# Optimization experiments

Measured on AMD Instinct MI355X. Metric: run time of the kernel, lower is better.

## Reference

```python
import math
import jax, jax.numpy as jnp
import numpy as np


def _tril_colmajor_index(d):
    # Maps packed icf tail entries (column-by-column, strictly lower) to (r, c).
    idx = np.zeros((d, d), dtype=np.int32)
    p = 0
    for c in range(d):
        for r in range(c + 1, d):
            idx[r, c] = p
            p += 1
    mask = np.tri(d, d, -1, dtype=bool)  # strictly lower triangular
    return idx, mask


def setup_inputs() -> dict:
    key = jax.random.key(0)
    k1, k2, k3, k4 = jax.random.split(key, 4)
    K, d, N = 64, 32, 50000
    icf_cols = d + d * (d - 1) // 2  # 528
    return {
        "alphas": jax.random.normal(k1, (K,), dtype=jnp.float32),
        "means": jax.random.normal(k2, (K, d), dtype=jnp.float32),
        "icf": jax.random.normal(k3, (K, icf_cols), dtype=jnp.float32),
        "x": jax.random.normal(k4, (N, d), dtype=jnp.float32),
        "wishart_gamma": jnp.ones((), dtype=jnp.float32),
        "wishart_m": jnp.ones((), dtype=jnp.float32),
    }


def reference(alphas, means, icf, x, wishart_gamma, wishart_m):
    n, d = x.shape
    k = alphas.shape[0]
    idx, mask = _tril_colmajor_index(d)
    idx = jnp.asarray(idx)
    mask = jnp.asarray(mask)

    Qdiags = jnp.exp(icf[:, :d])            # [K, d]
    sum_qs = jnp.sum(icf[:, :d], axis=1)    # [K]
    Ltail = icf[:, d:]                      # [K, d(d-1)/2]
    # Vectorized constructL: strictly-lower triangular L per component. [K, d, d]
    L = jnp.where(mask[None], Ltail[:, idx], jnp.zeros((), icf.dtype))

    xc = x[:, None, :] - means[None, :, :]  # [N, K, d]
    # Qtimesx: diag scaling + batched triangular matvec
    Lx = Qdiags[None] * xc + jnp.einsum('kij,nkj->nki', L, xc)  # [N, K, d]
    sqsum = jnp.sum(Lx * Lx, axis=2)        # [N, K]

    inner = alphas[None, :] + sum_qs[None, :] - 0.5 * sqsum
    slse = jnp.sum(jax.scipy.special.logsumexp(inner, axis=1))

    CONSTANT = -n * d * 0.5 * math.log(2 * math.pi)

    # log_wishart_prior
    nw = d + wishart_m + 1.0
    out_w = jnp.sum(0.5 * wishart_gamma * wishart_gamma
                    * (jnp.sum(Qdiags ** 2, axis=1) + jnp.sum(Ltail ** 2, axis=1))
                    - wishart_m * sum_qs)
    C = nw * d * jnp.log(wishart_gamma / math.sqrt(2.0))
    prior = out_w - k * (C - jax.scipy.special.multigammaln(0.5 * nw, d))

    return CONSTANT + slse - n * jax.scipy.special.logsumexp(alphas) + prior
```

## Files before the change

kernel.cpp:

```cpp
#include <hip/hip_runtime.h>
#include <math.h>
#include <utility>

#define K_COMP 64
#define D 32
#define NTRIL 496
#define ICF_COLS 528
#define NPAIR 528
#define NFEAT 560
#define NCHUNK 18
#define PTS_PER_BLK 32
#define ROWB 1168

typedef __attribute__((ext_vector_type(8))) short v8s;
typedef __attribute__((ext_vector_type(4))) float v4f;

__device__ __forceinline__ unsigned short f2bf(float f) {
  unsigned int u = __float_as_uint(f);
  unsigned int r = (u + 0x7FFFu + ((u >> 16) & 1u)) >> 16;
  return (unsigned short)r;
}
__device__ __forceinline__ v8s asv8(int4 v) {
  union { int4 i; v8s s; } u; u.i = v; return u.s;
}

constexpr int pr_i(int t) { int i = 0; while (t >= D - i) { t -= D - i; ++i; } return i; }
constexpr int pr_j(int t) { int i = 0; while (t >= D - i) { t -= D - i; ++i; } return i + t; }

template<int F> __device__ __forceinline__ float feat(const float (&xr)[D]) {
  if constexpr (F < 32) return xr[F];
  else if constexpr (F < NFEAT) {
    constexpr int t = F - 32, i = pr_i(t), j = pr_j(t);
    return xr[i] * xr[j];
  } else return 0.0f;
}

template<int F0> __device__ __forceinline__ void write4(const float (&xr)[D], char* row) {
  unsigned int d0 = (unsigned int)f2bf(feat<F0+0>(xr)) | ((unsigned int)f2bf(feat<F0+1>(xr)) << 16);
  unsigned int d1 = (unsigned int)f2bf(feat<F0+2>(xr)) | ((unsigned int)f2bf(feat<F0+3>(xr)) << 16);
  *reinterpret_cast<uint2*>(row + (size_t)F0 * 2) = make_uint2(d0, d1);
}
template<int BASE, size_t... Qs> __device__ __forceinline__
void gen72(const float (&xr)[D], char* row, std::index_sequence<Qs...>) {
  (write4<BASE + 4 * (int)Qs>(xr, row), ...);
}

__global__ __launch_bounds__(64) void gmm_prep(
    const float* __restrict__ alphas, const float* __restrict__ means,
    const float* __restrict__ icf, const float* __restrict__ wg,
    const float* __restrict__ wm,
    uint4* __restrict__ Whi, float* __restrict__ eSa, float* __restrict__ wwk)
{
  int k = blockIdx.x;
  int l = threadIdx.x;
  __shared__ float M[D][D + 1];
  __shared__ float mu[D], b[D], v[D];
  __shared__ float At[NPAIR];
  __shared__ float red[64];

  const float* ick = icf + (size_t)k * ICF_COLS;

  if (l < D) {
    mu[l] = means[k * D + l];
    float q = __expf(ick[l]);
    for (int c = 0; c < D; ++c) {
      float val;
      if (c < l) { int off = c * 31 - c * (c - 1) / 2; val = ick[D + off + (l - c - 1)]; }
      else if (c == l) val = q;
      else val = 0.0f;
      M[l][c] = val;
    }
  }
  __syncthreads();
  if (l < D) {
    float acc = 0.f;
    for (int c = 0; c < D; ++c) acc = fmaf(M[l][c], mu[c], acc);
    b[l] = acc;
  }
  __syncthreads();
  if (l < D) {
    float acc = 0.f;
    for (int r = 0; r < D; ++r) acc = fmaf(M[r][l], b[r], acc);
    v[l] = acc;
  }
  for (int t = l; t < NPAIR; t += 64) {
    int tt = t, i = 0;
    while (tt >= D - i) { tt -= D - i; ++i; }
    int j = i + tt;
    float acc = 0.f;
    for (int r = 0; r < D; ++r) acc = fmaf(M[r][i], M[r][j], acc);
    At[t] = (i == j) ? -0.5f * acc : -acc;
  }
  float part = 0.f;
  for (int e = l; e < D * D; e += 64) {
    float mv = M[e / D][e % D];
    part = fmaf(mv, mv, part);
  }
  red[l] = part;
  __syncthreads();
  for (int st = 32; st > 0; st >>= 1) {
    if (l < st) red[l] += red[l + st];
    __syncthreads();
  }
  if (l == 0) {
    float msq = red[0];
    float sumq = 0.f;
    for (int i = 0; i < D; ++i) sumq += ick[i];
    float bsq = 0.f;
    for (int i = 0; i < D; ++i) bsq = fmaf(b[i], b[i], bsq);
    eSa[k] = alphas[k] + sumq - 0.5f * bsq;
    float g = wg[0], mm = wm[0];
    wwk[k] = 0.5f * g * g * msq - mm * sumq;
  }
  __syncthreads();

  int s = k >> 4, krow = k & 15;
  for (int u = l; u < NCHUNK * 4; u += 64) {
    int c = u >> 2, g = u & 3;
    unsigned int hw[4] = {0, 0, 0, 0};
    for (int j2 = 0; j2 < 8; ++j2) {
      int f = c * 32 + g * 8 + j2;
      float wv2;
      if (f < 32) wv2 = v[f];
      else if (f < NFEAT) wv2 = At[f - 32];
      else wv2 = 0.0f;
      hw[j2 >> 1] |= ((unsigned int)f2bf(wv2)) << (16 * (j2 & 1));
    }
    Whi[(s * NCHUNK + c) * 64 + g * 16 + krow] = make_uint4(hw[0], hw[1], hw[2], hw[3]);
  }
}

__global__ __launch_bounds__(256) void gmm_main(
    const float* __restrict__ x, const int4* __restrict__ Whi,
    const float* __restrict__ eSa, int N, float* __restrict__ partials)
{
  __shared__ __align__(16) char phi[PTS_PER_BLK * ROWB];
  __shared__ float lmm[4][PTS_PER_BLK];
  __shared__ float lss[4][PTS_PER_BLK];

  int tid = threadIdx.x;
  int lane = tid & 63;

  {
    int ptl = tid & 31;
    int h = tid >> 5;
    int n = blockIdx.x * PTS_PER_BLK + ptl;
    int nn = (n < N) ? n : (N - 1);
    float xr[D];
    const float4* xp = reinterpret_cast<const float4*>(x + (size_t)nn * D);
#pragma unroll
    for (int i = 0; i < D / 4; ++i) {
      float4 vv = xp[i];
      xr[4 * i + 0] = vv.x; xr[4 * i + 1] = vv.y; xr[4 * i + 2] = vv.z; xr[4 * i + 3] = vv.w;
    }
    char* row = phi + (size_t)ptl * ROWB;
    switch (h) {
      case 0: gen72<  0>(xr, row, std::make_index_sequence<18>{}); break;
      case 1: gen72< 72>(xr, row, std::make_index_sequence<18>{}); break;
      case 2: gen72<144>(xr, row, std::make_index_sequence<18>{}); break;
      case 3: gen72<216>(xr, row, std::make_index_sequence<18>{}); break;
      case 4: gen72<288>(xr, row, std::make_index_sequence<18>{}); break;
      case 5: gen72<360>(xr, row, std::make_index_sequence<18>{}); break;
      case 6: gen72<432>(xr, row, std::make_index_sequence<18>{}); break;
      case 7: gen72<504>(xr, row, std::make_index_sequence<18>{}); break;
    }
  }
  __syncthreads();

  int slice = __builtin_amdgcn_readfirstlane(tid >> 6);
  int g = lane >> 4, n16 = lane & 15;

  v4f acc0 = {0.f, 0.f, 0.f, 0.f};
  v4f acc1 = {0.f, 0.f, 0.f, 0.f};
  const char* brow0 = phi + (size_t)(0 * 16 + n16) * ROWB + g * 16;
  const char* brow1 = phi + (size_t)(1 * 16 + n16) * ROWB + g * 16;

#pragma unroll
  for (int c = 0; c < NCHUNK; ++c) {
    int4 ah = Whi[(slice * NCHUNK + c) * 64 + lane];
    int4 b0 = *reinterpret_cast<const int4*>(brow0 + c * 64);
    int4 b1 = *reinterpret_cast<const int4*>(brow1 + c * 64);
    v8s ahs = asv8(ah), b0s = asv8(b0), b1s = asv8(b1);
    acc0 = __builtin_amdgcn_mfma_f32_16x16x32_bf16(ahs, b0s, acc0, 0, 0, 0);
    acc1 = __builtin_amdgcn_mfma_f32_16x16x32_bf16(ahs, b1s, acc1, 0, 0, 0);
  }

  float4 es = reinterpret_cast<const float4*>(eSa)[slice * 4 + (lane >> 4)];
  acc0.x += es.x; acc0.y += es.y; acc0.z += es.z; acc0.w += es.w;
  acc1.x += es.x; acc1.y += es.y; acc1.z += es.z; acc1.w += es.w;

#pragma unroll
  for (int G = 0; G < 2; ++G) {
    v4f a = (G == 0) ? acc0 : acc1;
    float m = fmaxf(fmaxf(a.x, a.y), fmaxf(a.z, a.w));
    float sv = __expf(a.x - m) + __expf(a.y - m) + __expf(a.z - m) + __expf(a.w - m);
#pragma unroll
    for (int off = 16; off <= 32; off <<= 1) {
      float mo = __shfl_xor(m, off);
      float so = __shfl_xor(sv, off);
      float mn = fmaxf(m, mo);
      sv = sv * __expf(m - mn) + so * __expf(mo - mn);
      m = mn;
    }
    if (lane < 16) { lmm[slice][G * 16 + lane] = m; lss[slice][G * 16 + lane] = sv; }
  }
  __syncthreads();

  if (tid < PTS_PER_BLK) {
    float m0 = lmm[0][tid], m1 = lmm[1][tid], m2 = lmm[2][tid], m3 = lmm[3][tid];
    float mm = fmaxf(fmaxf(m0, m1), fmaxf(m2, m3));
    float ss = lss[0][tid] * __expf(m0 - mm) + lss[1][tid] * __expf(m1 - mm)
             + lss[2][tid] * __expf(m2 - mm) + lss[3][tid] * __expf(m3 - mm);
    int n = blockIdx.x * PTS_PER_BLK + tid;
    float lse = (n < N) ? (mm + __logf(ss)) : 0.f;
#pragma unroll
    for (int off = 16; off > 0; off >>= 1) lse += __shfl_down(lse, off);
    if (tid == 0) partials[blockIdx.x] = lse;
  }
}

__global__ __launch_bounds__(256) void gmm_final(
    const float* __restrict__ wwk, const float* __restrict__ partials, int nblocks,
    const float* __restrict__ alphas, const float* __restrict__ wg,
    const float* __restrict__ wm, int N, float* __restrict__ out)
{
  int tid = threadIdx.x;
  __shared__ double sd[256];
  __shared__ float samax;
  __shared__ double s_slse, s_sa, s_ow;

  double acc = 0.0;
  for (int i = tid; i < nblocks; i += 256) acc += (double)partials[i];
  sd[tid] = acc;
  __syncthreads();
  for (int st = 128; st > 0; st >>= 1) {
    if (tid < st) sd[tid] += sd[tid + st];
    __syncthreads();
  }
  if (tid == 0) s_slse = sd[0];
  __syncthreads();

  if (tid < 64) {
    float m = alphas[tid];
#pragma unroll
    for (int off = 32; off > 0; off >>= 1) m = fmaxf(m, __shfl_xor(m, off));
    if (tid == 0) samax = m;
  }
  __syncthreads();

  sd[tid] = (tid < K_COMP) ? exp((double)(alphas[tid] - samax)) : 0.0;
  __syncthreads();
  for (int st = 128; st > 0; st >>= 1) {
    if (tid < st) sd[tid] += sd[tid + st];
    __syncthreads();
  }
  if (tid == 0) s_sa = sd[0];
  __syncthreads();

  sd[tid] = (tid < K_COMP) ? (double)wwk[tid] : 0.0;
  __syncthreads();
  for (int st = 128; st > 0; st >>= 1) {
    if (tid < st) sd[tid] += sd[tid + st];
    __syncthreads();
  }
  if (tid == 0) s_ow = sd[0];
  __syncthreads();

  double nw = (double)D + (double)wm[0] + 1.0;
  sd[tid] = (tid < D) ? lgamma(0.5 * nw + (1.0 - (double)(tid + 1)) * 0.5) : 0.0;
  __syncthreads();
  for (int st = 128; st > 0; st >>= 1) {
    if (tid < st) sd[tid] += sd[tid + st];
    __syncthreads();
  }

  if (tid == 0) {
    double mg = (D * (D - 1) / 4.0) * log(M_PI) + sd[0];
    double lse_a = (double)samax + log(s_sa);
    double g = (double)wg[0];
    double C = nw * (double)D * log(g / sqrt(2.0));
    double CONST = -(double)N * D * 0.5 * log(2.0 * M_PI);
    double prior = s_ow - (double)K_COMP * (C - mg);
    out[0] = (float)(CONST + s_slse - (double)N * lse_a + prior);
  }
}

extern "C" void kernel_launch(void* const* d_in, const int* in_sizes, int n_in,
                              void* d_out, int out_size, void* d_ws, size_t ws_size,
                              hipStream_t stream)
{
  const float* alphas = (const float*)d_in[0];
  const float* means  = (const float*)d_in[1];
  const float* icf    = (const float*)d_in[2];
  const float* x      = (const float*)d_in[3];
  const float* wg     = (const float*)d_in[4];
  const float* wm     = (const float*)d_in[5];
  float* out = (float*)d_out;

  int N = in_sizes[3] / D;
  int npblk = (N + PTS_PER_BLK - 1) / PTS_PER_BLK;

  char* wsb = (char*)d_ws;
  const size_t WBYTES = (size_t)4 * NCHUNK * 64 * 16;
  uint4* Whi = (uint4*)wsb;
  float* eSa = (float*)(wsb + WBYTES);
  float* wwk = eSa + K_COMP;
  float* partials = wwk + K_COMP;

  gmm_prep<<<K_COMP, 64, 0, stream>>>(alphas, means, icf, wg, wm, Whi, eSa, wwk);
  gmm_main<<<npblk, 256, 0, stream>>>(x, (const int4*)Whi, eSa, N, partials);
  gmm_final<<<1, 256, 0, stream>>>(wwk, partials, npblk, alphas, wg, wm, N, out);
}
```

Measured before the change: 42.29 us.

## Build quadratic features in registers with full symmetric Gram matrix per wave

Replaces the shared-memory packed upper-triangle feature table with on-the-fly generation of x_a*x_b products in registers, using the full symmetric 32x32 matrix (scaled by -0.5) plus a linear chunk, for 33 K-chunks. Each wave now handles 32 points against all 64 components (4 slices), so the cross-wave LDS logsumexp reduction and block barrier go away, and A fragments are software-prefetched from global. This removes LDS traffic and syncs at the cost of nearly double the MFMA work (33 vs 18 chunks per slice) and per-chunk scalar x loads.

```diff
diff --git a/kernel.cpp b/kernel.cpp
--- a/kernel.cpp
+++ b/kernel.cpp
@@ -1,16 +1,11 @@
 #include <hip/hip_runtime.h>
 #include <math.h>
-#include <utility>
 
 #define K_COMP 64
 #define D 32
-#define NTRIL 496
 #define ICF_COLS 528
-#define NPAIR 528
-#define NFEAT 560
-#define NCHUNK 18
-#define PTS_PER_BLK 32
-#define ROWB 1168
+#define NCH 33
+#define SLICES 4
 
 typedef __attribute__((ext_vector_type(8))) short v8s;
 typedef __attribute__((ext_vector_type(4))) float v4f;
@@ -20,42 +15,25 @@
   unsigned int r = (u + 0x7FFFu + ((u >> 16) & 1u)) >> 16;
   return (unsigned short)r;
 }
+__device__ __forceinline__ v8s pack8(unsigned a, unsigned b, unsigned c, unsigned d) {
+  union { unsigned u[4]; v8s s; } u;
+  u.u[0] = a; u.u[1] = b; u.u[2] = c; u.u[3] = d; return u.s;
+}
 __device__ __forceinline__ v8s asv8(int4 v) {
   union { int4 i; v8s s; } u; u.i = v; return u.s;
-}
-
-constexpr int pr_i(int t) { int i = 0; while (t >= D - i) { t -= D - i; ++i; } return i; }
-constexpr int pr_j(int t) { int i = 0; while (t >= D - i) { t -= D - i; ++i; } return i + t; }
-
-template<int F> __device__ __forceinline__ float feat(const float (&xr)[D]) {
-  if constexpr (F < 32) return xr[F];
-  else if constexpr (F < NFEAT) {
-    constexpr int t = F - 32, i = pr_i(t), j = pr_j(t);
-    return xr[i] * xr[j];
-  } else return 0.0f;
-}
-
-template<int F0> __device__ __forceinline__ void write4(const float (&xr)[D], char* row) {
-  unsigned int d0 = (unsigned int)f2bf(feat<F0+0>(xr)) | ((unsigned int)f2bf(feat<F0+1>(xr)) << 16);
-  unsigned int d1 = (unsigned int)f2bf(feat<F0+2>(xr)) | ((unsigned int)f2bf(feat<F0+3>(xr)) << 16);
-  *reinterpret_cast<uint2*>(row + (size_t)F0 * 2) = make_uint2(d0, d1);
-}
-template<int BASE, size_t... Qs> __device__ __forceinline__
-void gen72(const float (&xr)[D], char* row, std::index_sequence<Qs...>) {
-  (write4<BASE + 4 * (int)Qs>(xr, row), ...);
 }
 
 __global__ __launch_bounds__(64) void gmm_prep(
     const float* __restrict__ alphas, const float* __restrict__ means,
     const float* __restrict__ icf, const float* __restrict__ wg,
     const float* __restrict__ wm,
-    uint4* __restrict__ Whi, float* __restrict__ eSa, float* __restrict__ wwk)
+    uint4* __restrict__ W2, float* __restrict__ eSa, float* __restrict__ wwk)
 {
   int k = blockIdx.x;
   int l = threadIdx.x;
   __shared__ float M[D][D + 1];
   __shared__ float mu[D], b[D], v[D];
-  __shared__ float At[NPAIR];
+  __shared__ float Afl[D * D];
   __shared__ float red[64];
 
   const float* ick = icf + (size_t)k * ICF_COLS;
@@ -83,13 +61,11 @@
     for (int r = 0; r < D; ++r) acc = fmaf(M[r][l], b[r], acc);
     v[l] = acc;
   }
-  for (int t = l; t < NPAIR; t += 64) {
-    int tt = t, i = 0;
-    while (tt >= D - i) { tt -= D - i; ++i; }
-    int j = i + tt;
+  for (int e = l; e < D * D; e += 64) {
+    int a = e >> 5, bb = e & 31;
     float acc = 0.f;
-    for (int r = 0; r < D; ++r) acc = fmaf(M[r][i], M[r][j], acc);
-    At[t] = (i == j) ? -0.5f * acc : -acc;
+    for (int r = 0; r < D; ++r) acc = fmaf(M[r][a], M[r][bb], acc);
+    Afl[e] = -0.5f * acc;
   }
   float part = 0.f;
   for (int e = l; e < D * D; e += 64) {
@@ -115,85 +91,105 @@
   __syncthreads();
 
   int s = k >> 4, krow = k & 15;
-  for (int u = l; u < NCHUNK * 4; u += 64) {
+  for (int u = l; u < NCH * 4; u += 64) {
     int c = u >> 2, g = u & 3;
     unsigned int hw[4] = {0, 0, 0, 0};
     for (int j2 = 0; j2 < 8; ++j2) {
-      int f = c * 32 + g * 8 + j2;
-      float wv2;
-      if (f < 32) wv2 = v[f];
-      else if (f < NFEAT) wv2 = At[f - 32];
-      else wv2 = 0.0f;
-      hw[j2 >> 1] |= ((unsigned int)f2bf(wv2)) << (16 * (j2 & 1));
-    }
-    Whi[(s * NCHUNK + c) * 64 + g * 16 + krow] = make_uint4(hw[0], hw[1], hw[2], hw[3]);
-  }
-}
-
-__global__ __launch_bounds__(256) void gmm_main(
-    const float* __restrict__ x, const int4* __restrict__ Whi,
+      int bb = g * 8 + j2;
+      float val = (c < D) ? Afl[c * 32 + bb] : v[bb];
+      hw[j2 >> 1] |= ((unsigned int)f2bf(val)) << (16 * (j2 & 1));
+    }
+    W2[(s * NCH + c) * 64 + g * 16 + krow] = make_uint4(hw[0], hw[1], hw[2], hw[3]);
+  }
+}
+
+__global__ __launch_bounds__(256, 4) void gmm_main(
+    const float* __restrict__ x, const int4* __restrict__ W2,
     const float* __restrict__ eSa, int N, float* __restrict__ partials)
 {
-  __shared__ __align__(16) char phi[PTS_PER_BLK * ROWB];
-  __shared__ float lmm[4][PTS_PER_BLK];
-  __shared__ float lss[4][PTS_PER_BLK];
-
   int tid = threadIdx.x;
   int lane = tid & 63;
-
+  int wv = tid >> 6;
+  int w = blockIdx.x * 4 + wv;
+  int n16 = lane & 15, g = lane >> 4;
+
+  int pt0 = (2 * w) * 16 + n16;
+  int pt1 = (2 * w + 1) * 16 + n16;
+  bool pv0 = pt0 < N, pv1 = pt1 < N;
+  const float* xr0 = x + (size_t)(pv0 ? pt0 : (N - 1)) * D;
+  const float* xr1 = x + (size_t)(pv1 ? pt1 : (N - 1)) * D;
+
+  int bb = g * 8;
+  float xb0[8], xb1[8];
   {
-    int ptl = tid & 31;
-    int h = tid >> 5;
-    int n = blockIdx.x * PTS_PER_BLK + ptl;
-    int nn = (n < N) ? n : (N - 1);
-    float xr[D];
-    const float4* xp = reinterpret_cast<const float4*>(x + (size_t)nn * D);
-#pragma unroll
-    for (int i = 0; i < D / 4; ++i) {
-      float4 vv = xp[i];
-      xr[4 * i + 0] = vv.x; xr[4 * i + 1] = vv.y; xr[4 * i + 2] = vv.z; xr[4 * i + 3] = vv.w;
-    }
-    char* row = phi + (size_t)ptl * ROWB;
-    switch (h) {
-      case 0: gen72<  0>(xr, row, std::make_index_sequence<18>{}); break;
-      case 1: gen72< 72>(xr, row, std::make_index_sequence<18>{}); break;
-      case 2: gen72<144>(xr, row, std::make_index_sequence<18>{}); break;
-      case 3: gen72<216>(xr, row, std::make_index_sequence<18>{}); break;
-      case 4: gen72<288>(xr, row, std::make_index_sequence<18>{}); break;
-      case 5: gen72<360>(xr, row, std::make_index_sequence<18>{}); break;
-      case 6: gen72<432>(xr, row, std::make_index_sequence<18>{}); break;
-      case 7: gen72<504>(xr, row, std::make_index_sequence<18>{}); break;
-    }
-  }
-  __syncthreads();
-
-  int slice = __builtin_amdgcn_readfirstlane(tid >> 6);
-  int g = lane >> 4, n16 = lane & 15;
-
-  v4f acc0 = {0.f, 0.f, 0.f, 0.f};
-  v4f acc1 = {0.f, 0.f, 0.f, 0.f};
-  const char* brow0 = phi + (size_t)(0 * 16 + n16) * ROWB + g * 16;
-  const char* brow1 = phi + (size_t)(1 * 16 + n16) * ROWB + g * 16;
-
-#pragma unroll
-  for (int c = 0; c < NCHUNK; ++c) {
-    int4 ah = Whi[(slice * NCHUNK + c) * 64 + lane];
-    int4 b0 = *reinterpret_cast<const int4*>(brow0 + c * 64);
-    int4 b1 = *reinterpret_cast<const int4*>(brow1 + c * 64);
-    v8s ahs = asv8(ah), b0s = asv8(b0), b1s = asv8(b1);
-    acc0 = __builtin_amdgcn_mfma_f32_16x16x32_bf16(ahs, b0s, acc0, 0, 0, 0);
-    acc1 = __builtin_amdgcn_mfma_f32_16x16x32_bf16(ahs, b1s, acc1, 0, 0, 0);
-  }
-
-  float4 es = reinterpret_cast<const float4*>(eSa)[slice * 4 + (lane >> 4)];
-  acc0.x += es.x; acc0.y += es.y; acc0.z += es.z; acc0.w += es.w;
-  acc1.x += es.x; acc1.y += es.y; acc1.z += es.z; acc1.w += es.w;
-
-#pragma unroll
-  for (int G = 0; G < 2; ++G) {
-    v4f a = (G == 0) ? acc0 : acc1;
-    float m = fmaxf(fmaxf(a.x, a.y), fmaxf(a.z, a.w));
-    float sv = __expf(a.x - m) + __expf(a.y - m) + __expf(a.z - m) + __expf(a.w - m);
+    float4 a0 = *reinterpret_cast<const float4*>(xr0 + bb);
+    float4 a1 = *reinterpret_cast<const float4*>(xr0 + bb + 4);
+    float4 c0 = *reinterpret_cast<const float4*>(xr1 + bb);
+    float4 c1 = *reinterpret_cast<const float4*>(xr1 + bb + 4);
+    xb0[0]=a0.x; xb0[1]=a0.y; xb0[2]=a0.z; xb0[3]=a0.w;
+    xb0[4]=a1.x; xb0[5]=a1.y; xb0[6]=a1.z; xb0[7]=a1.w;
+    xb1[0]=c0.x; xb1[1]=c0.y; xb1[2]=c0.z; xb1[3]=c0.w;
+    xb1[4]=c1.x; xb1[5]=c1.y; xb1[6]=c1.z; xb1[7]=c1.w;
+  }
+
+  const int4* wp = W2 + lane;
+  v4f acc[2][SLICES];
+#pragma unroll
+  for (int t = 0; t < 2; ++t)
+#pragma unroll
+    for (int s = 0; s < SLICES; ++s) acc[t][s] = (v4f){0.f, 0.f, 0.f, 0.f};
+
+  int4 Ac[SLICES], An[SLICES];
+#pragma unroll
+  for (int s = 0; s < SLICES; ++s) Ac[s] = wp[(s * NCH) * 64];
+
+#pragma unroll 1
+  for (int c = 0; c < NCH; ++c) {
+    if (c + 1 < NCH) {
+#pragma unroll
+      for (int s = 0; s < SLICES; ++s) An[s] = wp[(s * NCH + c + 1) * 64];
+    }
+    float xa0 = 1.0f, xa1 = 1.0f;
+    if (c < D) { xa0 = xr0[c]; xa1 = xr1[c]; }
+
+    unsigned d0[4], d1[4];
+#pragma unroll
+    for (int q = 0; q < 4; ++q) {
+      d0[q] = (unsigned)f2bf(xa0 * xb0[2*q]) | ((unsigned)f2bf(xa0 * xb0[2*q+1]) << 16);
+      d1[q] = (unsigned)f2bf(xa1 * xb1[2*q]) | ((unsigned)f2bf(xa1 * xb1[2*q+1]) << 16);
+    }
+    v8s B0 = pack8(d0[0], d0[1], d0[2], d0[3]);
+    v8s B1 = pack8(d1[0], d1[1], d1[2], d1[3]);
+
+#pragma unroll
+    for (int s = 0; s < SLICES; ++s) {
+      v8s As = asv8(Ac[s]);
+      acc[0][s] = __builtin_amdgcn_mfma_f32_16x16x32_bf16(As, B0, acc[0][s], 0, 0, 0);
+      acc[1][s] = __builtin_amdgcn_mfma_f32_16x16x32_bf16(As, B1, acc[1][s], 0, 0, 0);
+    }
+#pragma unroll
+    for (int s = 0; s < SLICES; ++s) Ac[s] = An[s];
+  }
+
+  const float4* esp = reinterpret_cast<const float4*>(eSa);
+  float tsum[2];
+#pragma unroll
+  for (int t = 0; t < 2; ++t) {
+    float vals[16];
+#pragma unroll
+    for (int s = 0; s < SLICES; ++s) {
+      float4 es = esp[s * 4 + g];
+      vals[s*4+0] = acc[t][s].x + es.x;
+      vals[s*4+1] = acc[t][s].y + es.y;
+      vals[s*4+2] = acc[t][s].z + es.z;
+      vals[s*4+3] = acc[t][s].w + es.w;
+    }
+    float m = vals[0];
+#pragma unroll
+    for (int i = 1; i < 16; ++i) m = fmaxf(m, vals[i]);
+    float sv = 0.f;
+#pragma unroll
+    for (int i = 0; i < 16; ++i) sv += __expf(vals[i] - m);
 #pragma unroll
     for (int off = 16; off <= 32; off <<= 1) {
       float mo = __shfl_xor(m, off);
@@ -202,25 +198,17 @@
       sv = sv * __expf(m - mn) + so * __expf(mo - mn);
       m = mn;
     }
-    if (lane < 16) { lmm[slice][G * 16 + lane] = m; lss[slice][G * 16 + lane] = sv; }
-  }
-  __syncthreads();
-
-  if (tid < PTS_PER_BLK) {
-    float m0 = lmm[0][tid], m1 = lmm[1][tid], m2 = lmm[2][tid], m3 = lmm[3][tid];
-    float mm = fmaxf(fmaxf(m0, m1), fmaxf(m2, m3));
-    float ss = lss[0][tid] * __expf(m0 - mm) + lss[1][tid] * __expf(m1 - mm)
-             + lss[2][tid] * __expf(m2 - mm) + lss[3][tid] * __expf(m3 - mm);
-    int n = blockIdx.x * PTS_PER_BLK + tid;
-    float lse = (n < N) ? (mm + __logf(ss)) : 0.f;
-#pragma unroll
-    for (int off = 16; off > 0; off >>= 1) lse += __shfl_down(lse, off);
-    if (tid == 0) partials[blockIdx.x] = lse;
-  }
+    bool pv = (t == 0) ? pv0 : pv1;
+    float lse = pv ? (m + __logf(sv)) : 0.f;
+#pragma unroll
+    for (int off = 8; off > 0; off >>= 1) lse += __shfl_down(lse, off);
+    tsum[t] = lse;
+  }
+  if (lane == 0) partials[w] = tsum[0] + tsum[1];
 }
 
 __global__ __launch_bounds__(256) void gmm_final(
-    const float* __restrict__ wwk, const float* __restrict__ partials, int nblocks,
+    const float* __restrict__ wwk, const float* __restrict__ partials, int nparts,
     const float* __restrict__ alphas, const float* __restrict__ wg,
     const float* __restrict__ wm, int N, float* __restrict__ out)
 {
@@ -230,7 +218,7 @@
   __shared__ double s_slse, s_sa, s_ow;
 
   double acc = 0.0;
-  for (int i = tid; i < nblocks; i += 256) acc += (double)partials[i];
+  for (int i = tid; i < nparts; i += 256) acc += (double)partials[i];
   sd[tid] = acc;
   __syncthreads();
   for (int st = 128; st > 0; st >>= 1) {
@@ -298,16 +286,19 @@
   float* out = (float*)d_out;
 
   int N = in_sizes[3] / D;
-  int npblk = (N + PTS_PER_BLK - 1) / PTS_PER_BLK;
+  int ntiles = (N + 15) / 16;
+  int nwaves = (ntiles + 1) / 2;
+  int nblk   = (nwaves + 3) / 4;
+  int nparts = nblk * 4;
 
   char* wsb = (char*)d_ws;
-  const size_t WBYTES = (size_t)4 * NCHUNK * 64 * 16;
-  uint4* Whi = (uint4*)wsb;
-  float* eSa = (float*)(wsb + WBYTES);
+  const size_t W2BYTES = (size_t)SLICES * NCH * 64 * 16;
+  uint4* W2  = (uint4*)wsb;
+  float* eSa = (float*)(wsb + W2BYTES);
   float* wwk = eSa + K_COMP;
   float* partials = wwk + K_COMP;
 
-  gmm_prep<<<K_COMP, 64, 0, stream>>>(alphas, means, icf, wg, wm, Whi, eSa, wwk);
-  gmm_main<<<npblk, 256, 0, stream>>>(x, (const int4*)Whi, eSa, N, partials);
-  gmm_final<<<1, 256, 0, stream>>>(wwk, partials, npblk, alphas, wg, wm, N, out);
-}
+  gmm_prep<<<K_COMP, 64, 0, stream>>>(alphas, means, icf, wg, wm, W2, eSa, wwk);
+  gmm_main<<<nblk, 256, 0, stream>>>(x, (const int4*)W2, eSa, N, partials);
+  gmm_final<<<1, 256, 0, stream>>>(wwk, partials, nparts, alphas, wg, wm, N, out);
+}
```

After: 48.95 us. +15.7%, slower.
